# Kernel optimization log

Hardware: AMD Instinct MI355X
Metric: run time of the kernel (lower is better)

Reference implementation:

```python
import jax, jax.numpy as jnp
import numpy as np

ROT = 256  # Hadamard block size (ConvLinear4bit._n)


def _hadamard(n):
    # Sylvester construction of the n x n Hadamard matrix (n power of 2)
    H = np.array([[1.0]], dtype=np.float32)
    while H.shape[0] < n:
        H = np.block([[H, H], [H, -H]])
    return jnp.asarray(H / np.sqrt(n), dtype=jnp.float32)


def setup_inputs() -> dict:
    key = jax.random.key(0)
    k1, k2, k3, k4 = jax.random.split(key, 4)
    N, D_in, D_out = 4096, 4096, 4096
    x = jax.random.normal(k1, (N, D_in), dtype=jnp.float32)
    # unpacked int4 weights in [-7, 7] (logical content of the packed uint8 buffer)
    weight_int = jax.random.randint(k2, (D_out, D_in), -7, 8, dtype=jnp.int32)
    # per-output-row weight scales (quarot: max|W_rot| / 7)
    w_scale = jax.random.uniform(k3, (D_out, 1), dtype=jnp.float32) * 0.01 + 1e-4
    bias = jax.random.normal(k4, (D_out,), dtype=jnp.float32) * 0.01
    return {"x": x, "weight_int": weight_int, "w_scale": w_scale, "bias": bias}


def reference(x, weight_int, w_scale, bias):
    N, D = x.shape
    H = _hadamard(ROT)
    # blockwise Hadamard rotation along the feature dim (D is a multiple of ROT)
    x_rot = (x.reshape(N, D // ROT, ROT) @ H).reshape(N, D)
    # per-row symmetric int4 quantization of activations
    scales_x = jnp.max(jnp.abs(x_rot), axis=-1, keepdims=True) / 7.0  # [N, 1]
    q_x = jnp.clip(jnp.round(x_rot / scales_x), -8, 7).astype(jnp.int32)
    acc = jnp.matmul(q_x, weight_int.T)
    # sym_dequant: row scale (activations) * col scale (weights), then bias
    out = acc.astype(jnp.float32) * scales_x * w_scale.T + bias
    return out
```

## Files before the change

### kernel.cpp

```cpp
#include <hip/hip_runtime.h>
#include <math.h>

typedef int v4i __attribute__((ext_vector_type(4)));

#define DIM 4096
#define BT 128
#define KT 128

__device__ __forceinline__ void async16(const void* g, void* l) {
    __builtin_amdgcn_global_load_lds((__attribute__((address_space(1))) void*)(g),
                                     (__attribute__((address_space(3))) void*)(l),
                                     16, 0, 0);
}

__global__ __launch_bounds__(256) void wconv(const int* __restrict__ w,
                                             signed char* __restrict__ w8) {
    int i = blockIdx.x * 256 + threadIdx.x;
    int4 v = ((const int4*)w)[i];
    char4 c;
    c.x = (signed char)v.x; c.y = (signed char)v.y;
    c.z = (signed char)v.z; c.w = (signed char)v.w;
    ((char4*)w8)[i] = c;
}

__global__ __launch_bounds__(256) void rotquant(const float* __restrict__ x,
                                                signed char* __restrict__ q,
                                                float* __restrict__ scales) {
    const int row  = blockIdx.x;
    const int lane = threadIdx.x & 63;
    const int wave = threadIdx.x >> 6;
    const float4* xr4 = (const float4*)(x + (size_t)row * DIM);

    float sgn[6];
    #pragma unroll
    for (int i = 0; i < 6; ++i) sgn[i] = (lane & (1 << i)) ? -1.0f : 1.0f;

    float f[4][4];
    #pragma unroll
    for (int b = 0; b < 4; ++b) {
        const int blk = wave + 4 * b;
        float4 v = xr4[blk * 64 + lane];
        float t0 = v.x + v.y, t1 = v.x - v.y;
        float t2 = v.z + v.w, t3 = v.z - v.w;
        f[b][0] = t0 + t2; f[b][1] = t1 + t3;
        f[b][2] = t0 - t2; f[b][3] = t1 - t3;
        #pragma unroll
        for (int st = 0; st < 6; ++st) {
            const int m = 1 << st;
            #pragma unroll
            for (int j = 0; j < 4; ++j) {
                float p = __shfl_xor(f[b][j], m, 64);
                f[b][j] = fmaf(sgn[st], f[b][j], p);
            }
        }
        #pragma unroll
        for (int j = 0; j < 4; ++j) f[b][j] *= 0.0625f;
    }

    float m = 0.0f;
    #pragma unroll
    for (int b = 0; b < 4; ++b)
        #pragma unroll
        for (int j = 0; j < 4; ++j) m = fmaxf(m, fabsf(f[b][j]));
    #pragma unroll
    for (int d = 32; d; d >>= 1) m = fmaxf(m, __shfl_xor(m, d, 64));
    __shared__ float sm[4];
    if (lane == 0) sm[wave] = m;
    __syncthreads();
    m = fmaxf(fmaxf(sm[0], sm[1]), fmaxf(sm[2], sm[3]));

    const float s = m / 7.0f;
    if (threadIdx.x == 0) scales[row] = s;

    char4* qr4 = (char4*)(q + (size_t)row * DIM);
    #pragma unroll
    for (int b = 0; b < 4; ++b) {
        const int blk = wave + 4 * b;
        char4 c;
        int qi;
        qi = (int)rintf(f[b][0] / s); c.x = (signed char)min(7, max(-8, qi));
        qi = (int)rintf(f[b][1] / s); c.y = (signed char)min(7, max(-8, qi));
        qi = (int)rintf(f[b][2] / s); c.z = (signed char)min(7, max(-8, qi));
        qi = (int)rintf(f[b][3] / s); c.w = (signed char)min(7, max(-8, qi));
        qr4[blk * 64 + lane] = c;
    }
}

__global__ __launch_bounds__(256) void gemm_q8(const signed char* __restrict__ A,
                                               const signed char* __restrict__ B,
                                               const float* __restrict__ rowScale,
                                               const float* __restrict__ wscale,
                                               const float* __restrict__ bias,
                                               float* __restrict__ out) {
    __shared__ __align__(16) signed char As[BT * KT];
    __shared__ __align__(16) signed char Bs[BT * KT];

    const int bm = blockIdx.y, bn = blockIdx.x;
    const int t = threadIdx.x;
    const int lane = t & 63, wave = t >> 6;
    const int wm = (wave >> 1) * 64, wn = (wave & 1) * 64;
    const int quad = lane >> 4, mr = lane & 15;

    v4i acc[4][4] = {};

    for (int kt = 0; kt < DIM; kt += KT) {
        __syncthreads();
        #pragma unroll
        for (int h = 0; h < 4; ++h) {
            const int cidx = t + 256 * h;
            const int row  = cidx >> 3;
            const int g    = (cidx & 7) ^ (row & 7);
            async16(A + (size_t)(bm * BT + row) * DIM + kt + g * 16, &As[cidx * 16]);
            async16(B + (size_t)(bn * BT + row) * DIM + kt + g * 16, &Bs[cidx * 16]);
        }
        __syncthreads();

        #pragma unroll
        for (int s = 0; s < 2; ++s) {
            v4i a[4], b[4];
            #pragma unroll
            for (int i = 0; i < 4; ++i) {
                const int r = wm + i * 16 + mr;
                const int c = wn + i * 16 + mr;
                const int cl = s * 4 + quad;
                a[i] = *(const v4i*)&As[r * KT + ((cl ^ (r & 7)) * 16)];
                b[i] = *(const v4i*)&Bs[c * KT + ((cl ^ (c & 7)) * 16)];
            }
            #pragma unroll
            for (int i = 0; i < 4; ++i)
                #pragma unroll
                for (int j = 0; j < 4; ++j)
                    acc[i][j] = __builtin_amdgcn_mfma_i32_16x16x64_i8(a[i], b[j], acc[i][j], 0, 0, 0);
        }
    }

    #pragma unroll
    for (int j = 0; j < 4; ++j) {
        const int col = bn * BT + wn + j * 16 + mr;
        const float ws = wscale[col];
        const float bs = bias[col];
        #pragma unroll
        for (int i = 0; i < 4; ++i) {
            #pragma unroll
            for (int r = 0; r < 4; ++r) {
                const int row = bm * BT + wm + i * 16 + quad * 4 + r;
                out[(size_t)row * DIM + col] =
                    ((float)acc[i][j][r] * rowScale[row]) * ws + bs;
            }
        }
    }
}

extern "C" void kernel_launch(void* const* d_in, const int* in_sizes, int n_in,
                              void* d_out, int out_size, void* d_ws, size_t ws_size,
                              hipStream_t stream) {
    const float* x      = (const float*)d_in[0];
    const int*   wint   = (const int*)d_in[1];
    const float* wscale = (const float*)d_in[2];
    const float* bias   = (const float*)d_in[3];
    float* out = (float*)d_out;

    signed char* q8 = (signed char*)d_ws;
    signed char* w8 = q8 + (size_t)DIM * DIM;
    float* sx = (float*)(w8 + (size_t)DIM * DIM);

    wconv<<<(DIM * DIM / 4) / 256, 256, 0, stream>>>(wint, w8);
    rotquant<<<DIM, 256, 0, stream>>>(x, q8, sx);
    gemm_q8<<<dim3(DIM / BT, DIM / BT), 256, 0, stream>>>(q8, w8, sx, wscale, bias, out);
}
```

Baseline: 253.4 us.

## Switch GEMM to 32x32x32 int8 MFMA and fuse prep kernels

```diff
diff --git a/kernel.cpp b/kernel.cpp
--- a/kernel.cpp
+++ b/kernel.cpp
@@ -1,7 +1,8 @@
 #include <hip/hip_runtime.h>
 #include <math.h>
 
-typedef int v4i __attribute__((ext_vector_type(4)));
+typedef int v4i  __attribute__((ext_vector_type(4)));
+typedef int v16i __attribute__((ext_vector_type(16)));
 
 #define DIM 4096
 #define BT 128
@@ -13,19 +14,20 @@
                                      16, 0, 0);
 }
 
-__global__ __launch_bounds__(256) void wconv(const int* __restrict__ w,
-                                             signed char* __restrict__ w8) {
-    int i = blockIdx.x * 256 + threadIdx.x;
-    int4 v = ((const int4*)w)[i];
-    char4 c;
-    c.x = (signed char)v.x; c.y = (signed char)v.y;
-    c.z = (signed char)v.z; c.w = (signed char)v.w;
-    ((char4*)w8)[i] = c;
-}
-
-__global__ __launch_bounds__(256) void rotquant(const float* __restrict__ x,
-                                                signed char* __restrict__ q,
-                                                float* __restrict__ scales) {
+__global__ __launch_bounds__(256) void prep(const float* __restrict__ x,
+                                            const int* __restrict__ w,
+                                            signed char* __restrict__ q,
+                                            signed char* __restrict__ w8,
+                                            float* __restrict__ scales) {
+    if (blockIdx.x >= 4096) {
+        int i = (blockIdx.x - 4096) * 256 + threadIdx.x;
+        int4 v = ((const int4*)w)[i];
+        char4 c;
+        c.x = (signed char)v.x; c.y = (signed char)v.y;
+        c.z = (signed char)v.z; c.w = (signed char)v.w;
+        ((char4*)w8)[i] = c;
+        return;
+    }
     const int row  = blockIdx.x;
     const int lane = threadIdx.x & 63;
     const int wave = threadIdx.x >> 6;
@@ -99,51 +101,66 @@
     const int t = threadIdx.x;
     const int lane = t & 63, wave = t >> 6;
     const int wm = (wave >> 1) * 64, wn = (wave & 1) * 64;
-    const int quad = lane >> 4, mr = lane & 15;
+    const int l31 = lane & 31, lh = lane >> 5;
 
-    v4i acc[4][4] = {};
+    const signed char* ga[4];
+    const signed char* gb[4];
+    #pragma unroll
+    for (int h = 0; h < 4; ++h) {
+        const int cidx = t + 256 * h;
+        const int row  = cidx >> 3;
+        const int g    = (cidx & 7) ^ (row & 7);
+        ga[h] = A + (size_t)(bm * BT + row) * DIM + g * 16;
+        gb[h] = B + (size_t)(bn * BT + row) * DIM + g * 16;
+    }
+
+    const v4i* pa[2][4];
+    const v4i* pb[2][4];
+    #pragma unroll
+    for (int i = 0; i < 2; ++i)
+        #pragma unroll
+        for (int s = 0; s < 4; ++s) {
+            const int r  = wm + i * 32 + l31;
+            const int c  = wn + i * 32 + l31;
+            const int cl = 2 * s + lh;
+            pa[i][s] = (const v4i*)&As[r * KT + ((cl ^ (r & 7)) * 16)];
+            pb[i][s] = (const v4i*)&Bs[c * KT + ((cl ^ (c & 7)) * 16)];
+        }
+
+    v16i acc[2][2] = {};
 
     for (int kt = 0; kt < DIM; kt += KT) {
         __syncthreads();
         #pragma unroll
         for (int h = 0; h < 4; ++h) {
-            const int cidx = t + 256 * h;
-            const int row  = cidx >> 3;
-            const int g    = (cidx & 7) ^ (row & 7);
-            async16(A + (size_t)(bm * BT + row) * DIM + kt + g * 16, &As[cidx * 16]);
-            async16(B + (size_t)(bn * BT + row) * DIM + kt + g * 16, &Bs[cidx * 16]);
+            const int l = (t + 256 * h) * 16;
+            async16(ga[h], &As[l]); ga[h] += KT;
+            async16(gb[h], &Bs[l]); gb[h] += KT;
         }
         __syncthreads();
 
         #pragma unroll
-        for (int s = 0; s < 2; ++s) {
-            v4i a[4], b[4];
-            #pragma unroll
-            for (int i = 0; i < 4; ++i) {
-                const int r = wm + i * 16 + mr;
-                const int c = wn + i * 16 + mr;
-                const int cl = s * 4 + quad;
-                a[i] = *(const v4i*)&As[r * KT + ((cl ^ (r & 7)) * 16)];
-                b[i] = *(const v4i*)&Bs[c * KT + ((cl ^ (c & 7)) * 16)];
-            }
-            #pragma unroll
-            for (int i = 0; i < 4; ++i)
-                #pragma unroll
-                for (int j = 0; j < 4; ++j)
-                    acc[i][j] = __builtin_amdgcn_mfma_i32_16x16x64_i8(a[i], b[j], acc[i][j], 0, 0, 0);
+        for (int s = 0; s < 4; ++s) {
+            const v4i a0 = *pa[0][s], a1 = *pa[1][s];
+            const v4i b0 = *pb[0][s], b1 = *pb[1][s];
+            acc[0][0] = __builtin_amdgcn_mfma_i32_32x32x32_i8(a0, b0, acc[0][0], 0, 0, 0);
+            acc[0][1] = __builtin_amdgcn_mfma_i32_32x32x32_i8(a0, b1, acc[0][1], 0, 0, 0);
+            acc[1][0] = __builtin_amdgcn_mfma_i32_32x32x32_i8(a1, b0, acc[1][0], 0, 0, 0);
+            acc[1][1] = __builtin_amdgcn_mfma_i32_32x32x32_i8(a1, b1, acc[1][1], 0, 0, 0);
         }
     }
 
     #pragma unroll
-    for (int j = 0; j < 4; ++j) {
-        const int col = bn * BT + wn + j * 16 + mr;
+    for (int j = 0; j < 2; ++j) {
+        const int col = bn * BT + wn + j * 32 + l31;
         const float ws = wscale[col];
         const float bs = bias[col];
         #pragma unroll
-        for (int i = 0; i < 4; ++i) {
+        for (int i = 0; i < 2; ++i) {
+            const int rb = bm * BT + wm + i * 32 + 4 * lh;
             #pragma unroll
-            for (int r = 0; r < 4; ++r) {
-                const int row = bm * BT + wm + i * 16 + quad * 4 + r;
+            for (int r = 0; r < 16; ++r) {
+                const int row = rb + (r & 3) + 8 * (r >> 2);
                 out[(size_t)row * DIM + col] =
                     ((float)acc[i][j][r] * rowScale[row]) * ws + bs;
             }
@@ -164,7 +181,6 @@
     signed char* w8 = q8 + (size_t)DIM * DIM;
     float* sx = (float*)(w8 + (size_t)DIM * DIM);
 
-    wconv<<<(DIM * DIM / 4) / 256, 256, 0, stream>>>(wint, w8);
-    rotquant<<<DIM, 256, 0, stream>>>(x, q8, sx);
+    prep<<<4096 + 16384, 256, 0, stream>>>(x, wint, q8, w8, sx);
     gemm_q8<<<dim3(DIM / BT, DIM / BT), 256, 0, stream>>>(q8, w8, sx, wscale, bias, out);
 }
```

Result: faster. 242.4 us (-4.3%).
